# Kernel tuning notes

Measured on AMD Instinct MI355X. Metric: run time of the kernel, lower is better.

## Reference

```python
import jax, jax.numpy as jnp
import numpy as np


def _conv2d(x, w, b):
    # 3x3 conv, stride 1, pad 1, NCHW
    y = jax.lax.conv_general_dilated(x, w, (1, 1), ((1, 1), (1, 1)),
                                     dimension_numbers=('NCHW', 'OIHW', 'NCHW'))
    return y + b[None, :, None, None]


def _up2(x):
    return jnp.repeat(jnp.repeat(x, 2, axis=2), 2, axis=3)


def _mdconv(x, w, b, ow, ob):
    # Modulated deformable conv v2 (mmcv semantics): 3x3, stride 1, pad 1,
    # dilation 1, deformable_groups=1. Offsets/mask predicted by conv_offset,
    # out = chunk3 -> (o1, o2, mask); offset = cat(o1, o2); mask = sigmoid(mask).
    B, Cin, H, W = x.shape
    off = _conv2d(x, ow, ob)                        # [B,27,H,W]
    o1, o2, m = jnp.split(off, 3, axis=1)
    offs = jnp.concatenate([o1, o2], axis=1)        # [B,18,H,W]
    dy, dx = offs[:, 0::2], offs[:, 1::2]           # [B,9,H,W] (dy,dx interleaved per kernel pt)
    mask = jax.nn.sigmoid(m)                        # [B,9,H,W]
    ky, kx = jnp.meshgrid(jnp.arange(3), jnp.arange(3), indexing='ij')
    # sampling positions: p0 + pn + offset (pad=1)
    py = jnp.arange(H, dtype=x.dtype)[None, None, :, None] - 1.0 + ky.reshape(1, 9, 1, 1) + dy
    px = jnp.arange(W, dtype=x.dtype)[None, None, None, :] - 1.0 + kx.reshape(1, 9, 1, 1) + dx
    y0 = jnp.floor(py); x0 = jnp.floor(px)
    wy1 = py - y0; wx1 = px - x0
    y0i = y0.astype(jnp.int32); x0i = x0.astype(jnp.int32)
    flat = x.reshape(B, Cin, H * W)

    def gather(yi, xi):
        valid = ((yi >= 0) & (yi < H) & (xi >= 0) & (xi < W)).astype(x.dtype)  # zero padding
        idx = jnp.clip(yi, 0, H - 1) * W + jnp.clip(xi, 0, W - 1)             # [B,9,H,W]
        g = jax.vmap(lambda f, i: f[:, i])(flat, idx)                          # [B,Cin,9,H,W]
        return g * valid[:, None]

    val = (gather(y0i, x0i) * ((1 - wy1) * (1 - wx1))[:, None]
           + gather(y0i, x0i + 1) * ((1 - wy1) * wx1)[:, None]
           + gather(y0i + 1, x0i) * (wy1 * (1 - wx1))[:, None]
           + gather(y0i + 1, x0i + 1) * (wy1 * wx1)[:, None])
    cols = val * mask[:, None]                      # [B,Cin,9,H,W]
    out = jnp.einsum('ock,bckhw->bohw', w.reshape(w.shape[0], Cin, 9), cols)
    return out + b[None, :, None, None]


def setup_inputs() -> dict:
    key = jax.random.key(0)
    ks = jax.random.split(key, 24)
    C = 256
    sizes = [(96, 96), (48, 48), (24, 24), (12, 12)]
    d = {}
    for i, (h, w) in enumerate(sizes):
        d[f'x{i}'] = jax.random.normal(ks[i], (2, C, h, w), dtype=jnp.float32)
    for i in range(4):
        d[f'w{i}'] = jax.random.normal(ks[4 + i], (C, C, 3, 3), dtype=jnp.float32) * 0.02
        d[f'b{i}'] = jax.random.normal(ks[8 + i], (C,), dtype=jnp.float32) * 0.02
    for i in range(1, 4):
        d[f'ow{i}'] = jax.random.normal(ks[12 + i], (27, C, 3, 3), dtype=jnp.float32) * 0.01
        d[f'ob{i}'] = jax.random.normal(ks[16 + i], (27,), dtype=jnp.float32) * 0.01
    return d


def reference(x0, x1, x2, x3, w0, w1, w2, w3, b0, b1, b2, b3,
              ow1, ow2, ow3, ob1, ob2, ob3):
    # tdm_convs[3] called with level=1 -> deform; the same-size nearest interpolate is identity
    t3 = _mdconv(x3, w3, b3, ow3, ob3)
    # i=3: tdm_convs[2](2, x2 + up(t3)) -> deform
    t2 = _mdconv(x2 + _up2(t3), w2, b2, ow2, ob2)
    # i=2: tdm_convs[1](1, x1 + up(t2)) -> deform
    t1 = _mdconv(x1 + _up2(t2), w1, b1, ow1, ob1)
    # i=1: tdm_convs[0](0, x0 + up(t1)) -> level 0 < start_level -> plain conv
    t0 = _conv2d(x0 + _up2(t1), w0, b0)
    return (t0, t1, t2, t3)
```

## Files before the change

### kernel.cpp

```cpp
#include <hip/hip_runtime.h>
#include <math.h>

__device__ __forceinline__ ushort f2bf(float f) {
    unsigned int u = __float_as_uint(f);
    u += 0x7FFFu + ((u >> 16) & 1u);
    return (ushort)(u >> 16);
}

typedef __attribute__((address_space(1))) const unsigned int guint;
typedef __attribute__((address_space(3))) unsigned int luint;
__device__ __forceinline__ void gload_lds16(const void* g, void* l) {
    __builtin_amdgcn_global_load_lds((guint*)g, (luint*)l, 16, 0, 0);
}

using bfrag = __attribute__((ext_vector_type(8))) short;
using f4    = __attribute__((ext_vector_type(4))) float;

__device__ __forceinline__ void bf8_to_f(uint4 v, float* o) {
    unsigned int u[4] = {v.x, v.y, v.z, v.w};
    #pragma unroll
    for (int i = 0; i < 4; ++i) {
        o[2 * i]     = __uint_as_float(u[i] << 16);
        o[2 * i + 1] = __uint_as_float(u[i] & 0xFFFF0000u);
    }
}

struct CvtArgs {
    const float* src[7];
    ushort*      dst[7];
    int          m[7];
};
__global__ __launch_bounds__(256) void cvt_kernel(CvtArgs a) {
    int t = blockIdx.y;
    int idx = blockIdx.x * 256 + threadIdx.x;
    int M = a.m[t];
    if (idx >= M * 288) return;
    int m = idx / 288, rem = idx - m * 288;
    int r = rem >> 5, c8 = rem & 31;
    const float* s = a.src[t] + ((size_t)(m * 256 + c8 * 8)) * 9 + r;
    ushort vals[8];
    #pragma unroll
    for (int j = 0; j < 8; ++j) vals[j] = f2bf(s[j * 9]);
    *(uint4*)&a.dst[t][(size_t)m * 2304 + r * 256 + c8 * 8] = *(uint4*)vals;
}

struct FillArgs {
    float* outp[3];
    const float* bias[3];
    int HW[3];
    float* zbase;
    int z4;
};
__global__ __launch_bounds__(256) void fill_kernel(FillArgs a) {
    int y = blockIdx.y;
    int i = blockIdx.x * 256 + threadIdx.x;
    if (y < 3) {
        int HW = a.HW[y];
        int total4 = (2 * 256 * HW) >> 2;
        if (i < total4) {
            int e = i << 2;
            int m = (e / HW) & 255;
            float v = a.bias[y][m];
            *(float4*)&a.outp[y][e] = float4{v, v, v, v};
        }
    } else {
        if (i < a.z4) ((float4*)a.zbase)[i] = float4{0.f, 0.f, 0.f, 0.f};
    }
}

__global__ __launch_bounds__(256) void xs_nhwc(
    const float* __restrict__ x, const float* __restrict__ prev,
    ushort* __restrict__ xs, int H, int W)
{
    __shared__ ushort tile[32][72];
    const int HW = H * W, W2 = W >> 1;
    int b = blockIdx.z, c0 = blockIdx.y * 32, hw0 = blockIdx.x * 64;
    const float* xb = x + ((size_t)b * 256 + c0) * HW;
    const float* pb = prev ? prev + ((size_t)b * 256 + c0) * (HW >> 2) : nullptr;

    int hwl = threadIdx.x & 63, cl0 = threadIdx.x >> 6;
    int hw = hw0 + hwl;
    bool ok = hw < HW;
    int hwc = ok ? hw : HW - 1;
    int h = hwc / W, w = hwc - h * W;
    int pidx = (h >> 1) * W2 + (w >> 1);
    #pragma unroll
    for (int p = 0; p < 8; ++p) {
        int cl = p * 4 + cl0;
        float v = 0.f;
        if (ok) {
            v = xb[(size_t)cl * HW + hw];
            if (pb) v += pb[(size_t)cl * (HW >> 2) + pidx];
        }
        tile[cl][hwl] = f2bf(v);
    }
    __syncthreads();
    int hwl2 = threadIdx.x >> 2, cc = (threadIdx.x & 3) * 8;
    int hw2 = hw0 + hwl2;
    if (hw2 < HW) {
        ushort vals[8];
        #pragma unroll
        for (int j = 0; j < 8; ++j) vals[j] = tile[cc + j][hwl2];
        *(uint4*)&xs[((size_t)b * HW + hw2) * 256 + c0 + cc] = *(uint4*)vals;
    }
}

__global__ __launch_bounds__(256) void off_mfma(
    const ushort* __restrict__ A, const ushort* __restrict__ xs,
    const ushort* __restrict__ zeros, float* __restrict__ offbuf,
    int N, int H, int W, int ktiles)
{
    __shared__ __align__(16) ushort As[2][32 * 32];
    __shared__ __align__(16) ushort Bs[2][64 * 32];
    const int b  = blockIdx.z;
    const int n0 = blockIdx.x * 64;
    const int kt0 = blockIdx.y * ktiles * 32;
    const int tid = threadIdx.x, lane = tid & 63, wv = tid >> 6;
    const ushort* xb = xs + (size_t)b * N * 256;

    int n = n0 + (tid >> 2); if (n >= N) n = N - 1;
    int h = n / W, w = n - h * W;
    int kcc = (tid & 3) * 8;

    auto stage = [&](int kt, int bi) {
        int r = kt >> 8, c0k = kt & 255;
        int ry = r / 3 - 1, rx = r - (r / 3) * 3 - 1;
        if (tid < 128) {
            int row = tid >> 2; if (row > 26) row = 26;
            gload_lds16(A + (size_t)row * 2304 + kt + kcc,
                        (char*)As[bi] + (size_t)(tid & ~63) * 16);
        }
        int ih = h + ry, iw = w + rx;
        const ushort* src = (ih >= 0 && ih < H && iw >= 0 && iw < W)
            ? xb + (((size_t)(ih * W + iw)) << 8) + c0k + kcc
            : zeros;
        gload_lds16(src, (char*)Bs[bi] + (size_t)(tid & ~63) * 16);
    };

    f4 acc[2] = {};
    stage(kt0, 0);
    for (int kk = 0; kk < ktiles; ++kk) {
        __syncthreads();
        if (kk + 1 < ktiles) stage(kt0 + (kk + 1) * 32, (kk + 1) & 1);
        const ushort* as = As[kk & 1];
        const ushort* bs = Bs[kk & 1];
        bfrag bf = *(const bfrag*)&bs[(wv * 16 + (lane & 15)) * 32 + (lane >> 4) * 8];
        bfrag a0 = *(const bfrag*)&as[(lane & 15) * 32 + (lane >> 4) * 8];
        bfrag a1 = *(const bfrag*)&as[(16 + (lane & 15)) * 32 + (lane >> 4) * 8];
        acc[0] = __builtin_amdgcn_mfma_f32_16x16x32_bf16(a0, bf, acc[0], 0, 0, 0);
        acc[1] = __builtin_amdgcn_mfma_f32_16x16x32_bf16(a1, bf, acc[1], 0, 0, 0);
    }

    int nn = n0 + wv * 16 + (lane & 15);
    if (nn < N) {
        #pragma unroll
        for (int mb = 0; mb < 2; ++mb)
            #pragma unroll
            for (int t = 0; t < 4; ++t) {
                int m = mb * 16 + (lane >> 4) * 4 + t;
                if (m < 27)
                    atomicAdd(&offbuf[((size_t)b * 27 + m) * N + nn], acc[mb][t]);
            }
    }
}

__global__ __launch_bounds__(256) void sampling_kernel(
    const ushort* __restrict__ xs, const float* __restrict__ off,
    const float* __restrict__ ob, ushort* __restrict__ cols,
    int H, int W)
{
    __shared__ float4 gw[32][9];
    __shared__ int4   go[32][9];
    const int HW = H * W;
    const int b = blockIdx.z;
    const int hw0 = blockIdx.x * 32;
    const int tid = threadIdx.x;
    const float* offb = off + (size_t)b * 27 * HW;
    const ushort* xb = xs + (size_t)b * HW * 256;

    for (int it = tid; it < 32 * 9; it += 256) {
        int hwl = it / 9, k = it - hwl * 9;
        int hw = hw0 + hwl; if (hw >= HW) hw = HW - 1;
        int h = hw / W, w = hw - h * W;
        float dy = offb[(size_t)(2 * k) * HW + hw] + ob[2 * k];
        float dx = offb[(size_t)(2 * k + 1) * HW + hw] + ob[2 * k + 1];
        float mv = offb[(size_t)(18 + k) * HW + hw] + ob[18 + k];
        float mk = 1.0f / (1.0f + __expf(-mv));
        float py = (float)h - 1.0f + (float)(k / 3) + dy;
        float px = (float)w - 1.0f + (float)(k % 3) + dx;
        float y0f = floorf(py), x0f = floorf(px);
        float wy = py - y0f, wx = px - x0f;
        int y0 = (int)y0f, x0i = (int)x0f;
        int y1 = y0 + 1, x1 = x0i + 1;
        bool vy0 = (y0 >= 0) & (y0 < H), vy1 = (y1 >= 0) & (y1 < H);
        bool vx0 = (x0i >= 0) & (x0i < W), vx1 = (x1 >= 0) & (x1 < W);
        float w00 = (1.f - wy) * (1.f - wx) * ((vy0 & vx0) ? mk : 0.f);
        float w01 = (1.f - wy) * wx        * ((vy0 & vx1) ? mk : 0.f);
        float w10 = wy * (1.f - wx)        * ((vy1 & vx0) ? mk : 0.f);
        float w11 = wy * wx                * ((vy1 & vx1) ? mk : 0.f);
        int cy0 = min(max(y0, 0), H - 1), cy1 = min(max(y1, 0), H - 1);
        int cx0 = min(max(x0i, 0), W - 1), cx1 = min(max(x1, 0), W - 1);
        gw[hwl][k] = float4{w00, w01, w10, w11};
        go[hwl][k] = int4{(cy0 * W + cx0) << 8, (cy0 * W + cx1) << 8,
                          (cy1 * W + cx0) << 8, (cy1 * W + cx1) << 8};
    }
    __syncthreads();

    int hwl = tid >> 3, cb = (tid & 7) * 32;
    int hw = hw0 + hwl;
    if (hw >= HW) return;
    ushort* colp = cols + ((size_t)b * HW + hw) * 2304 + cb;

    #pragma unroll
    for (int k = 0; k < 9; ++k) {
        float4 wv = gw[hwl][k];
        int4   ov = go[hwl][k];
        const ushort* p00 = xb + ov.x + cb;
        const ushort* p01 = xb + ov.y + cb;
        const ushort* p10 = xb + ov.z + cb;
        const ushort* p11 = xb + ov.w + cb;
        #pragma unroll
        for (int j = 0; j < 4; ++j) {
            float f00[8], f01[8], f10[8], f11[8];
            bf8_to_f(*(const uint4*)(p00 + 8 * j), f00);
            bf8_to_f(*(const uint4*)(p01 + 8 * j), f01);
            bf8_to_f(*(const uint4*)(p10 + 8 * j), f10);
            bf8_to_f(*(const uint4*)(p11 + 8 * j), f11);
            unsigned int pk[4];
            #pragma unroll
            for (int t = 0; t < 4; ++t) {
                float lo = f00[2 * t] * wv.x + f01[2 * t] * wv.y +
                           f10[2 * t] * wv.z + f11[2 * t] * wv.w;
                float hi = f00[2 * t + 1] * wv.x + f01[2 * t + 1] * wv.y +
                           f10[2 * t + 1] * wv.z + f11[2 * t + 1] * wv.w;
                pk[t] = (unsigned int)f2bf(lo) | ((unsigned int)f2bf(hi) << 16);
            }
            *(uint4*)(colp + k * 256 + 8 * j) = make_uint4(pk[0], pk[1], pk[2], pk[3]);
        }
    }
}

template<bool IMPLICIT, bool SPLITK>
__global__ __launch_bounds__(256) void mfma_gemm(
    const ushort* __restrict__ A, const float* __restrict__ bias,
    const ushort* __restrict__ Bt, const ushort* __restrict__ zeros,
    float* __restrict__ outp, int N, int H, int W, int kchunk)
{
    __shared__ __align__(16) ushort As[128 * 64];
    __shared__ __align__(16) ushort Bs[64 * 64];
    const int b  = blockIdx.z;
    const int m0 = (blockIdx.y & 1) * 128;
    const int kt0 = (blockIdx.y >> 1) * kchunk;
    const int n0 = blockIdx.x * 64;
    const int tid  = threadIdx.x;
    const int lane = tid & 63;
    const int wv   = tid >> 6;
    const int wm = wv & 1, wn = wv >> 1;

    const ushort* Bb = IMPLICIT ? Bt + (size_t)b * N * 256
                                : Bt + (size_t)b * (size_t)N * 2304;

    const int sc8 = ((tid & 7) ^ ((tid >> 3) & 7)) * 8;
    int bn[2], bh[2], bw[2];
    #pragma unroll
    for (int j = 0; j < 2; ++j) {
        int n = n0 + j * 32 + (tid >> 3); if (n >= N) n = N - 1;
        bn[j] = n; bh[j] = n / W; bw[j] = n - bh[j] * W;
    }

    auto stage = [&](int kt) {
        #pragma unroll
        for (int i = 0; i < 4; ++i) {
            int row = i * 32 + (tid >> 3);
            gload_lds16(A + (size_t)(m0 + row) * 2304 + kt + sc8,
                        (char*)As + (size_t)(i * 256 + (tid & ~63)) * 16);
        }
        if (!IMPLICIT) {
            #pragma unroll
            for (int j = 0; j < 2; ++j)
                gload_lds16(Bb + (size_t)bn[j] * 2304 + kt + sc8,
                            (char*)Bs + (size_t)(j * 256 + (tid & ~63)) * 16);
        } else {
            int r = kt >> 8, c0k = kt & 255;
            int ry = r / 3 - 1, rx = r - (r / 3) * 3 - 1;
            #pragma unroll
            for (int j = 0; j < 2; ++j) {
                int ih = bh[j] + ry, iw = bw[j] + rx;
                const ushort* src = (ih >= 0 && ih < H && iw >= 0 && iw < W)
                    ? Bb + (((size_t)(ih * W + iw)) << 8) + c0k + sc8
                    : zeros;
                gload_lds16(src, (char*)Bs + (size_t)(j * 256 + (tid & ~63)) * 16);
            }
        }
    };

    const int fq = (lane >> 4);
    const int fv = (lane & 7);
    f4 acc[4][2] = {};

    const int kend = kt0 + kchunk;
    for (int kt = kt0; kt < kend; kt += 64) {
        stage(kt);
        __syncthreads();
        bfrag af[2][4], bf[2][2];
        #pragma unroll
        for (int kh = 0; kh < 2; ++kh) {
            int ch = ((kh * 4 + fq) ^ fv) * 8;
            #pragma unroll
            for (int i = 0; i < 4; ++i) {
                int r = wm * 64 + i * 16 + (lane & 15);
                af[kh][i] = *(const bfrag*)&As[r * 64 + ch];
            }
            #pragma unroll
            for (int j = 0; j < 2; ++j) {
                int r = wn * 32 + j * 16 + (lane & 15);
                bf[kh][j] = *(const bfrag*)&Bs[r * 64 + ch];
            }
        }
        #pragma unroll
        for (int kh = 0; kh < 2; ++kh)
            #pragma unroll
            for (int i = 0; i < 4; ++i)
                #pragma unroll
                for (int j = 0; j < 2; ++j)
                    acc[i][j] = __builtin_amdgcn_mfma_f32_16x16x32_bf16(
                        af[kh][i], bf[kh][j], acc[i][j], 0, 0, 0);
        __syncthreads();
    }

    const int mb = m0 + wm * 64, nb = n0 + wn * 32;
    #pragma unroll
    for (int i = 0; i < 4; ++i) {
        int mrow = mb + i * 16 + (lane >> 4) * 4;
        #pragma unroll
        for (int j = 0; j < 2; ++j) {
            int n = nb + j * 16 + (lane & 15);
            if (n < N) {
                #pragma unroll
                for (int t = 0; t < 4; ++t) {
                    int m = mrow + t;
                    if (SPLITK)
                        atomicAdd(&outp[((size_t)b * 256 + m) * N + n], acc[i][j][t]);
                    else
                        outp[((size_t)b * 256 + m) * N + n] = acc[i][j][t] + bias[m];
                }
            }
        }
    }
}

extern "C" void kernel_launch(void* const* d_in, const int* in_sizes, int n_in,
                              void* d_out, int out_size, void* d_ws, size_t ws_size,
                              hipStream_t stream)
{
    const float* x[4]   = {(const float*)d_in[0], (const float*)d_in[1],
                           (const float*)d_in[2], (const float*)d_in[3]};
    const float* wgt[4] = {(const float*)d_in[4], (const float*)d_in[6],
                           (const float*)d_in[8], (const float*)d_in[10]};
    const float* bia[4] = {(const float*)d_in[5], (const float*)d_in[7],
                           (const float*)d_in[9], (const float*)d_in[11]};
    const float* owt[4] = {nullptr, (const float*)d_in[12],
                           (const float*)d_in[14], (const float*)d_in[16]};
    const float* obv[4] = {nullptr, (const float*)d_in[13],
                           (const float*)d_in[15], (const float*)d_in[17]};

    const int B = 2;
    const int Hs[4] = {96, 48, 24, 12};
    const int HWs[4] = {96 * 96, 48 * 48, 24 * 24, 12 * 12};

    float* out = (float*)d_out;
    size_t outOff[4];
    outOff[0] = 0;
    outOff[1] = outOff[0] + (size_t)B * 256 * HWs[0];
    outOff[2] = outOff[1] + (size_t)B * 256 * HWs[1];
    outOff[3] = outOff[2] + (size_t)B * 256 * HWs[2];

    char* ws = (char*)d_ws;
    size_t off = 0;
    auto carve = [&](size_t bytes) { void* p = ws + off; off = (off + bytes + 255) & ~(size_t)255; return p; };
    ushort* wbf[4];
    ushort* owbf[4] = {nullptr, nullptr, nullptr, nullptr};
    for (int i = 0; i < 4; ++i) wbf[i] = (ushort*)carve((size_t)256 * 2304 * 2);
    for (int i = 1; i < 4; ++i) owbf[i] = (ushort*)carve((size_t)27 * 2304 * 2);
    ushort* cols = (ushort*)carve((size_t)B * HWs[1] * 2304 * 2);
    ushort* xsb[4];
    for (int i = 0; i < 4; ++i) xsb[i] = (ushort*)carve((size_t)B * 256 * HWs[i] * 2);
    int offElems = B * 27 * (HWs[1] + HWs[2] + HWs[3]);
    float* offbase = (float*)carve((size_t)offElems * 4 + 1024);
    ushort* zeros = (ushort*)(offbase + offElems);
    float* offbuf[4] = {nullptr,
                        offbase,
                        offbase + (size_t)B * 27 * HWs[1],
                        offbase + (size_t)B * 27 * (HWs[1] + HWs[2])};

    {
        CvtArgs a;
        a.src[0] = wgt[0]; a.src[1] = wgt[1]; a.src[2] = wgt[2]; a.src[3] = wgt[3];
        a.src[4] = owt[1]; a.src[5] = owt[2]; a.src[6] = owt[3];
        a.dst[0] = wbf[0]; a.dst[1] = wbf[1]; a.dst[2] = wbf[2]; a.dst[3] = wbf[3];
        a.dst[4] = owbf[1]; a.dst[5] = owbf[2]; a.dst[6] = owbf[3];
        for (int i = 0; i < 4; ++i) a.m[i] = 256;
        for (int i = 4; i < 7; ++i) a.m[i] = 27;
        dim3 grd((256 * 288 + 255) / 256, 7);
        cvt_kernel<<<grd, 256, 0, stream>>>(a);
    }
    {
        FillArgs a;
        for (int i = 0; i < 3; ++i) {
            a.outp[i] = out + outOff[i + 1]; a.bias[i] = bia[i + 1]; a.HW[i] = HWs[i + 1];
        }
        a.zbase = offbase;
        a.z4 = (offElems * 4 + 1024) / 16;
        int maxE = 2 * 256 * HWs[1] / 4;
        if (a.z4 > maxE) maxE = a.z4;
        dim3 grd((maxE + 255) / 256, 4);
        fill_kernel<<<grd, 256, 0, stream>>>(a);
    }
    {
        dim3 grd((HWs[3] + 63) / 64, 8, B);
        xs_nhwc<<<grd, 256, 0, stream>>>(x[3], nullptr, xsb[3], Hs[3], Hs[3]);
    }

    const int ktiles[4] = {0, 9, 6, 3};
    const int ksplit[4] = {1, 2, 6, 12};

    for (int lvl = 3; lvl >= 1; --lvl) {
        int H = Hs[lvl], W = H, HW = HWs[lvl];

        {
            dim3 grd((HW + 63) / 64, 72 / ktiles[lvl], B);
            off_mfma<<<grd, 256, 0, stream>>>(
                owbf[lvl], xsb[lvl], zeros, offbuf[lvl], HW, H, W, ktiles[lvl]);
        }
        {
            dim3 grd((HW + 31) / 32, 1, B);
            sampling_kernel<<<grd, 256, 0, stream>>>(
                xsb[lvl], offbuf[lvl], obv[lvl], cols, H, W);
        }
        {
            dim3 grd((HW + 63) / 64, 2 * ksplit[lvl], B);
            mfma_gemm<false, true><<<grd, 256, 0, stream>>>(
                wbf[lvl], bia[lvl], cols, zeros, out + outOff[lvl],
                HW, H, W, 2304 / ksplit[lvl]);
        }
        {
            int Hn = Hs[lvl - 1];
            dim3 grd((HWs[lvl - 1] + 63) / 64, 8, B);
            xs_nhwc<<<grd, 256, 0, stream>>>(
                x[lvl - 1], out + outOff[lvl], xsb[lvl - 1], Hn, Hn);
        }
    }

    {
        dim3 grd((HWs[0] + 63) / 64, 2, B);
        mfma_gemm<true, false><<<grd, 256, 0, stream>>>(
            wbf[0], bia[0], xsb[0], zeros, out + outOff[0],
            HWs[0], Hs[0], Hs[0], 2304);
    }
}
```

Measured before the change: 294.0 us.

## Double-buffer LDS in MFMA GEMM, shrink M tile to 64, retune split-K

The GEMM kernel now uses two LDS buffers so the next K-tile's global-to-LDS load is issued while MFMAs run on the current tile, and it drops one barrier per iteration. The M tile is halved from 128 to 64, giving four M blocks per batch, which doubles the grid and raises occupancy. Split-K factors for the smaller levels are reduced to cut atomic traffic. The cost is re-reading the B tile for each M block and doing less MFMA work per LDS fragment load.

New measurement: 297.0 us. About the same (+1.0%).

```diff
diff --git a/kernel.cpp b/kernel.cpp
--- a/kernel.cpp
+++ b/kernel.cpp
@@ -246,11 +246,11 @@
     const ushort* __restrict__ Bt, const ushort* __restrict__ zeros,
     float* __restrict__ outp, int N, int H, int W, int kchunk)
 {
-    __shared__ __align__(16) ushort As[128 * 64];
-    __shared__ __align__(16) ushort Bs[64 * 64];
+    __shared__ __align__(16) ushort As[2][64 * 64];
+    __shared__ __align__(16) ushort Bs[2][64 * 64];
     const int b  = blockIdx.z;
-    const int m0 = (blockIdx.y & 1) * 128;
-    const int kt0 = (blockIdx.y >> 1) * kchunk;
+    const int m0 = (blockIdx.y & 3) * 64;
+    const int kt0 = (blockIdx.y >> 2) * kchunk;
     const int n0 = blockIdx.x * 64;
     const int tid  = threadIdx.x;
     const int lane = tid & 63;
@@ -261,25 +261,25 @@
                                 : Bt + (size_t)b * (size_t)N * 2304;
 
     const int sc8 = ((tid & 7) ^ ((tid >> 3) & 7)) * 8;
+    const int srow = tid >> 3;
     int bn[2], bh[2], bw[2];
     #pragma unroll
     for (int j = 0; j < 2; ++j) {
-        int n = n0 + j * 32 + (tid >> 3); if (n >= N) n = N - 1;
+        int n = n0 + j * 32 + srow; if (n >= N) n = N - 1;
         bn[j] = n; bh[j] = n / W; bw[j] = n - bh[j] * W;
     }
 
-    auto stage = [&](int kt) {
-        #pragma unroll
-        for (int i = 0; i < 4; ++i) {
-            int row = i * 32 + (tid >> 3);
-            gload_lds16(A + (size_t)(m0 + row) * 2304 + kt + sc8,
-                        (char*)As + (size_t)(i * 256 + (tid & ~63)) * 16);
+    auto stage = [&](int kt, int bi) {
+        #pragma unroll
+        for (int i = 0; i < 2; ++i) {
+            gload_lds16(A + (size_t)(m0 + i * 32 + srow) * 2304 + kt + sc8,
+                        (char*)As[bi] + (size_t)(i * 256 + (tid & ~63)) * 16);
         }
         if (!IMPLICIT) {
             #pragma unroll
             for (int j = 0; j < 2; ++j)
                 gload_lds16(Bb + (size_t)bn[j] * 2304 + kt + sc8,
-                            (char*)Bs + (size_t)(j * 256 + (tid & ~63)) * 16);
+                            (char*)Bs[bi] + (size_t)(j * 256 + (tid & ~63)) * 16);
         } else {
             int r = kt >> 8, c0k = kt & 255;
             int ry = r / 3 - 1, rx = r - (r / 3) * 3 - 1;
@@ -289,48 +289,46 @@
                 const ushort* src = (ih >= 0 && ih < H && iw >= 0 && iw < W)
                     ? Bb + (((size_t)(ih * W + iw)) << 8) + c0k + sc8
                     : zeros;
-                gload_lds16(src, (char*)Bs + (size_t)(j * 256 + (tid & ~63)) * 16);
+                gload_lds16(src, (char*)Bs[bi] + (size_t)(j * 256 + (tid & ~63)) * 16);
             }
         }
     };
 
     const int fq = (lane >> 4);
     const int fv = (lane & 7);
-    f4 acc[4][2] = {};
-
-    const int kend = kt0 + kchunk;
-    for (int kt = kt0; kt < kend; kt += 64) {
-        stage(kt);
+    f4 acc[2][2] = {};
+
+    const int nit = kchunk >> 6;
+    stage(kt0, 0);
+    for (int it = 0; it < nit; ++it) {
         __syncthreads();
-        bfrag af[2][4], bf[2][2];
+        if (it + 1 < nit) stage(kt0 + (it + 1) * 64, (it + 1) & 1);
+        const ushort* as = As[it & 1];
+        const ushort* bs = Bs[it & 1];
+        bfrag af[2][2], bf[2][2];
         #pragma unroll
         for (int kh = 0; kh < 2; ++kh) {
             int ch = ((kh * 4 + fq) ^ fv) * 8;
             #pragma unroll
-            for (int i = 0; i < 4; ++i) {
-                int r = wm * 64 + i * 16 + (lane & 15);
-                af[kh][i] = *(const bfrag*)&As[r * 64 + ch];
-            }
-            #pragma unroll
-            for (int j = 0; j < 2; ++j) {
-                int r = wn * 32 + j * 16 + (lane & 15);
-                bf[kh][j] = *(const bfrag*)&Bs[r * 64 + ch];
-            }
+            for (int i = 0; i < 2; ++i)
+                af[kh][i] = *(const bfrag*)&as[(wm * 32 + i * 16 + (lane & 15)) * 64 + ch];
+            #pragma unroll
+            for (int j = 0; j < 2; ++j)
+                bf[kh][j] = *(const bfrag*)&bs[(wn * 32 + j * 16 + (lane & 15)) * 64 + ch];
         }
         #pragma unroll
         for (int kh = 0; kh < 2; ++kh)
             #pragma unroll
-            for (int i = 0; i < 4; ++i)
+            for (int i = 0; i < 2; ++i)
                 #pragma unroll
                 for (int j = 0; j < 2; ++j)
                     acc[i][j] = __builtin_amdgcn_mfma_f32_16x16x32_bf16(
                         af[kh][i], bf[kh][j], acc[i][j], 0, 0, 0);
-        __syncthreads();
-    }
-
-    const int mb = m0 + wm * 64, nb = n0 + wn * 32;
-    #pragma unroll
-    for (int i = 0; i < 4; ++i) {
+    }
+
+    const int mb = m0 + wm * 32, nb = n0 + wn * 32;
+    #pragma unroll
+    for (int i = 0; i < 2; ++i) {
         int mrow = mb + i * 16 + (lane >> 4) * 4;
         #pragma unroll
         for (int j = 0; j < 2; ++j) {
@@ -422,7 +420,7 @@
     }
 
     const int ktiles[4] = {0, 9, 6, 3};
-    const int ksplit[4] = {1, 2, 6, 12};
+    const int ksplit[4] = {1, 2, 4, 6};
 
     for (int lvl = 3; lvl >= 1; --lvl) {
         int H = Hs[lvl], W = H, HW = HWs[lvl];
@@ -438,7 +436,7 @@
                 xsb[lvl], offbuf[lvl], obv[lvl], cols, H, W);
         }
         {
-            dim3 grd((HW + 63) / 64, 2 * ksplit[lvl], B);
+            dim3 grd((HW + 63) / 64, 4 * ksplit[lvl], B);
             mfma_gemm<false, true><<<grd, 256, 0, stream>>>(
                 wbf[lvl], bia[lvl], cols, zeros, out + outOff[lvl],
                 HW, H, W, 2304 / ksplit[lvl]);
@@ -452,7 +450,7 @@
     }
 
     {
-        dim3 grd((HWs[0] + 63) / 64, 2, B);
+        dim3 grd((HWs[0] + 63) / 64, 4, B);
         mfma_gemm<true, false><<<grd, 256, 0, stream>>>(
             wbf[0], bia[0], xsb[0], zeros, out + outOff[0],
             HWs[0], Hs[0], Hs[0], 2304);
```

## Fuse all stages into one cooperative persistent kernel with grid syncs

Applied to the files above, without the earlier changes.

Replaces the sequence of about fifteen kernel launches with a single cooperative kernel of 512 persistent blocks. Each stage loops over virtual block indices and is separated from the next by grid.sync(), which removes per-launch overhead and the gaps between launches. The sampling stage is also reshaped to 8 pixels per block with one 8-channel chunk per thread, giving more blocks at small levels. The cost is grid-wide barriers and fixed occupancy: stages with few tiles leave most blocks idle, and large stages loop several times over the persistent blocks.

After: 1.021 ms. 3.47x slower.

```diff
diff --git a/kernel.cpp b/kernel.cpp
--- a/kernel.cpp
+++ b/kernel.cpp
@@ -1,5 +1,8 @@
 #include <hip/hip_runtime.h>
+#include <hip/hip_cooperative_groups.h>
 #include <math.h>
+
+namespace cg = cooperative_groups;
 
 __device__ __forceinline__ ushort f2bf(float f) {
     unsigned int u = __float_as_uint(f);
@@ -25,56 +28,65 @@
     }
 }
 
-struct CvtArgs {
-    const float* src[7];
-    ushort*      dst[7];
-    int          m[7];
+struct MegaArgs {
+    const float* x[4];
+    const float* wgt[4];
+    const float* bia[4];
+    const float* owt[4];
+    const float* obv[4];
+    ushort* wbf[4];
+    ushort* owbf[4];
+    ushort* cols;
+    ushort* xsb[4];
+    float*  offbuf[4];
+    ushort* zeros;
+    float*  zbase;
+    int     z4;
+    float*  out[4];
 };
-__global__ __launch_bounds__(256) void cvt_kernel(CvtArgs a) {
-    int t = blockIdx.y;
-    int idx = blockIdx.x * 256 + threadIdx.x;
-    int M = a.m[t];
-    if (idx >= M * 288) return;
-    int m = idx / 288, rem = idx - m * 288;
-    int r = rem >> 5, c8 = rem & 31;
-    const float* s = a.src[t] + ((size_t)(m * 256 + c8 * 8)) * 9 + r;
-    ushort vals[8];
-    #pragma unroll
-    for (int j = 0; j < 8; ++j) vals[j] = f2bf(s[j * 9]);
-    *(uint4*)&a.dst[t][(size_t)m * 2304 + r * 256 + c8 * 8] = *(uint4*)vals;
-}
-
-struct FillArgs {
-    float* outp[3];
-    const float* bias[3];
-    int HW[3];
-    float* zbase;
-    int z4;
-};
-__global__ __launch_bounds__(256) void fill_kernel(FillArgs a) {
-    int y = blockIdx.y;
-    int i = blockIdx.x * 256 + threadIdx.x;
+
+__device__ __forceinline__ void st_cvt(const MegaArgs& a, int vb) {
+    int t = vb / 288, bxi = vb - t * 288;
+    int M = (t < 4) ? 256 : 27;
+    const float* src = (t < 4) ? a.wgt[t] : a.owt[t - 3];
+    ushort* dst = (t < 4) ? a.wbf[t] : a.owbf[t - 3];
+    int idx = bxi * 256 + threadIdx.x;
+    if (idx < M * 288) {
+        int m = idx / 288, rem = idx - m * 288;
+        int r = rem >> 5, c8 = rem & 31;
+        const float* s = src + ((size_t)(m * 256 + c8 * 8)) * 9 + r;
+        ushort vals[8];
+        #pragma unroll
+        for (int j = 0; j < 8; ++j) vals[j] = f2bf(s[j * 9]);
+        *(uint4*)&dst[(size_t)m * 2304 + r * 256 + c8 * 8] = *(uint4*)vals;
+    }
+}
+
+__device__ __forceinline__ void st_fill(const MegaArgs& a, int vb) {
+    int y = vb / 1152, bxi = vb - y * 1152;
+    int i = bxi * 256 + threadIdx.x;
     if (y < 3) {
-        int HW = a.HW[y];
-        int total4 = (2 * 256 * HW) >> 2;
-        if (i < total4) {
+        int HW = (y == 0) ? 2304 : (y == 1) ? 576 : 144;
+        float* outp = a.out[y + 1];
+        const float* bias = a.bia[y + 1];
+        if (i < 128 * HW) {
             int e = i << 2;
             int m = (e / HW) & 255;
-            float v = a.bias[y][m];
-            *(float4*)&a.outp[y][e] = float4{v, v, v, v};
+            float v = bias[m];
+            *(float4*)&outp[e] = float4{v, v, v, v};
         }
     } else {
         if (i < a.z4) ((float4*)a.zbase)[i] = float4{0.f, 0.f, 0.f, 0.f};
     }
 }
 
-__global__ __launch_bounds__(256) void xs_nhwc(
+__device__ __forceinline__ void st_xs(char* smemc,
     const float* __restrict__ x, const float* __restrict__ prev,
-    ushort* __restrict__ xs, int H, int W)
+    ushort* __restrict__ xs, int H, int W, int bx, int by, int bz)
 {
-    __shared__ ushort tile[32][72];
+    ushort (*tile)[72] = (ushort(*)[72])smemc;
     const int HW = H * W, W2 = W >> 1;
-    int b = blockIdx.z, c0 = blockIdx.y * 32, hw0 = blockIdx.x * 64;
+    int b = bz, c0 = by * 32, hw0 = bx * 64;
     const float* xb = x + ((size_t)b * 256 + c0) * HW;
     const float* pb = prev ? prev + ((size_t)b * 256 + c0) * (HW >> 2) : nullptr;
 
@@ -103,19 +115,18 @@
         for (int j = 0; j < 8; ++j) vals[j] = tile[cc + j][hwl2];
         *(uint4*)&xs[((size_t)b * HW + hw2) * 256 + c0 + cc] = *(uint4*)vals;
     }
-}
-
-__global__ __launch_bounds__(256) void off_mfma(
+    __syncthreads();
+}
+
+__device__ __forceinline__ void st_off(char* smemc,
     const ushort* __restrict__ A, const ushort* __restrict__ xs,
     const ushort* __restrict__ zeros, float* __restrict__ offbuf,
-    int N, int H, int W, int ktiles)
+    int N, int H, int W, int ktiles, int bx, int by, int bz)
 {
-    __shared__ __align__(16) ushort As[2][32 * 32];
-    __shared__ __align__(16) ushort Bs[2][64 * 32];
-    const int b  = blockIdx.z;
-    const int n0 = blockIdx.x * 64;
-    const int kt0 = blockIdx.y * ktiles * 32;
-    const int tid = threadIdx.x, lane = tid & 63, wv = tid >> 6;
+    ushort* As0 = (ushort*)smemc;
+    ushort* Bs0 = (ushort*)(smemc + 4096);
+    const int b = bz, n0 = bx * 64, kt0 = by * ktiles * 32;
+    const int tid = threadIdx.x, lane = tid & 63, wvv = tid >> 6;
     const ushort* xb = xs + (size_t)b * N * 256;
 
     int n = n0 + (tid >> 2); if (n >= N) n = N - 1;
@@ -128,13 +139,13 @@
         if (tid < 128) {
             int row = tid >> 2; if (row > 26) row = 26;
             gload_lds16(A + (size_t)row * 2304 + kt + kcc,
-                        (char*)As[bi] + (size_t)(tid & ~63) * 16);
+                        (char*)(As0 + bi * 1024) + (size_t)(tid & ~63) * 16);
         }
         int ih = h + ry, iw = w + rx;
         const ushort* src = (ih >= 0 && ih < H && iw >= 0 && iw < W)
             ? xb + (((size_t)(ih * W + iw)) << 8) + c0k + kcc
             : zeros;
-        gload_lds16(src, (char*)Bs[bi] + (size_t)(tid & ~63) * 16);
+        gload_lds16(src, (char*)(Bs0 + bi * 2048) + (size_t)(tid & ~63) * 16);
     };
 
     f4 acc[2] = {};
@@ -142,16 +153,17 @@
     for (int kk = 0; kk < ktiles; ++kk) {
         __syncthreads();
         if (kk + 1 < ktiles) stage(kt0 + (kk + 1) * 32, (kk + 1) & 1);
-        const ushort* as = As[kk & 1];
-        const ushort* bs = Bs[kk & 1];
-        bfrag bf = *(const bfrag*)&bs[(wv * 16 + (lane & 15)) * 32 + (lane >> 4) * 8];
+        const ushort* as = As0 + (kk & 1) * 1024;
+        const ushort* bs = Bs0 + (kk & 1) * 2048;
+        bfrag bf = *(const bfrag*)&bs[(wvv * 16 + (lane & 15)) * 32 + (lane >> 4) * 8];
         bfrag a0 = *(const bfrag*)&as[(lane & 15) * 32 + (lane >> 4) * 8];
         bfrag a1 = *(const bfrag*)&as[(16 + (lane & 15)) * 32 + (lane >> 4) * 8];
         acc[0] = __builtin_amdgcn_mfma_f32_16x16x32_bf16(a0, bf, acc[0], 0, 0, 0);
         acc[1] = __builtin_amdgcn_mfma_f32_16x16x32_bf16(a1, bf, acc[1], 0, 0, 0);
     }
-
-    int nn = n0 + wv * 16 + (lane & 15);
+    __syncthreads();
+
+    int nn = n0 + wvv * 16 + (lane & 15);
     if (nn < N) {
         #pragma unroll
         for (int mb = 0; mb < 2; ++mb)
@@ -164,22 +176,20 @@
     }
 }
 
-__global__ __launch_bounds__(256) void sampling_kernel(
+__device__ __forceinline__ void st_samp(char* smemc,
     const ushort* __restrict__ xs, const float* __restrict__ off,
     const float* __restrict__ ob, ushort* __restrict__ cols,
-    int H, int W)
+    int H, int W, int bx, int bz)
 {
-    __shared__ float4 gw[32][9];
-    __shared__ int4   go[32][9];
+    float4* gw = (float4*)smemc;
+    int4*   go = (int4*)(smemc + 8 * 9 * 16);
     const int HW = H * W;
-    const int b = blockIdx.z;
-    const int hw0 = blockIdx.x * 32;
-    const int tid = threadIdx.x;
+    const int b = bz, hw0 = bx * 8, tid = threadIdx.x;
     const float* offb = off + (size_t)b * 27 * HW;
     const ushort* xb = xs + (size_t)b * HW * 256;
 
-    for (int it = tid; it < 32 * 9; it += 256) {
-        int hwl = it / 9, k = it - hwl * 9;
+    if (tid < 72) {
+        int hwl = tid / 9, k = tid - hwl * 9;
         int hw = hw0 + hwl; if (hw >= HW) hw = HW - 1;
         int h = hw / W, w = hw - h * W;
         float dy = offb[(size_t)(2 * k) * HW + hw] + ob[2 * k];
@@ -200,32 +210,25 @@
         float w11 = wy * wx                * ((vy1 & vx1) ? mk : 0.f);
         int cy0 = min(max(y0, 0), H - 1), cy1 = min(max(y1, 0), H - 1);
         int cx0 = min(max(x0i, 0), W - 1), cx1 = min(max(x1, 0), W - 1);
-        gw[hwl][k] = float4{w00, w01, w10, w11};
-        go[hwl][k] = int4{(cy0 * W + cx0) << 8, (cy0 * W + cx1) << 8,
-                          (cy1 * W + cx0) << 8, (cy1 * W + cx1) << 8};
+        gw[hwl * 9 + k] = float4{w00, w01, w10, w11};
+        go[hwl * 9 + k] = int4{(cy0 * W + cx0) << 8, (cy0 * W + cx1) << 8,
+                               (cy1 * W + cx0) << 8, (cy1 * W + cx1) << 8};
     }
     __syncthreads();
 
-    int hwl = tid >> 3, cb = (tid & 7) * 32;
+    int hwl = tid >> 5, cb = (tid & 31) * 8;
     int hw = hw0 + hwl;
-    if (hw >= HW) return;
-    ushort* colp = cols + ((size_t)b * HW + hw) * 2304 + cb;
-
-    #pragma unroll
-    for (int k = 0; k < 9; ++k) {
-        float4 wv = gw[hwl][k];
-        int4   ov = go[hwl][k];
-        const ushort* p00 = xb + ov.x + cb;
-        const ushort* p01 = xb + ov.y + cb;
-        const ushort* p10 = xb + ov.z + cb;
-        const ushort* p11 = xb + ov.w + cb;
-        #pragma unroll
-        for (int j = 0; j < 4; ++j) {
+    if (hw < HW) {
+        ushort* colp = cols + ((size_t)b * HW + hw) * 2304 + cb;
+        #pragma unroll
+        for (int k = 0; k < 9; ++k) {
+            float4 wv = gw[hwl * 9 + k];
+            int4   ov = go[hwl * 9 + k];
             float f00[8], f01[8], f10[8], f11[8];
-            bf8_to_f(*(const uint4*)(p00 + 8 * j), f00);
-            bf8_to_f(*(const uint4*)(p01 + 8 * j), f01);
-            bf8_to_f(*(const uint4*)(p10 + 8 * j), f10);
-            bf8_to_f(*(const uint4*)(p11 + 8 * j), f11);
+            bf8_to_f(*(const uint4*)(xb + ov.x + cb), f00);
+            bf8_to_f(*(const uint4*)(xb + ov.y + cb), f01);
+            bf8_to_f(*(const uint4*)(xb + ov.z + cb), f10);
+            bf8_to_f(*(const uint4*)(xb + ov.w + cb), f11);
             unsigned int pk[4];
             #pragma unroll
             for (int t = 0; t < 4; ++t) {
@@ -235,23 +238,25 @@
                            f10[2 * t + 1] * wv.z + f11[2 * t + 1] * wv.w;
                 pk[t] = (unsigned int)f2bf(lo) | ((unsigned int)f2bf(hi) << 16);
             }
-            *(uint4*)(colp + k * 256 + 8 * j) = make_uint4(pk[0], pk[1], pk[2], pk[3]);
-        }
-    }
+            *(uint4*)(colp + k * 256) = make_uint4(pk[0], pk[1], pk[2], pk[3]);
+        }
+    }
+    __syncthreads();
 }
 
 template<bool IMPLICIT, bool SPLITK>
-__global__ __launch_bounds__(256) void mfma_gemm(
+__device__ __forceinline__ void st_gemm(char* smemc,
     const ushort* __restrict__ A, const float* __restrict__ bias,
     const ushort* __restrict__ Bt, const ushort* __restrict__ zeros,
-    float* __restrict__ outp, int N, int H, int W, int kchunk)
+    float* __restrict__ outp, int N, int H, int W, int kchunk,
+    int bx, int by, int bz)
 {
-    __shared__ __align__(16) ushort As[128 * 64];
-    __shared__ __align__(16) ushort Bs[64 * 64];
-    const int b  = blockIdx.z;
-    const int m0 = (blockIdx.y & 1) * 128;
-    const int kt0 = (blockIdx.y >> 1) * kchunk;
-    const int n0 = blockIdx.x * 64;
+    ushort* As = (ushort*)smemc;
+    ushort* Bs = (ushort*)(smemc + 16384);
+    const int b  = bz;
+    const int m0 = (by & 1) * 128;
+    const int kt0 = (by >> 1) * kchunk;
+    const int n0 = bx * 64;
     const int tid  = threadIdx.x;
     const int lane = tid & 63;
     const int wv   = tid >> 6;
@@ -261,18 +266,18 @@
                                 : Bt + (size_t)b * (size_t)N * 2304;
 
     const int sc8 = ((tid & 7) ^ ((tid >> 3) & 7)) * 8;
+    const int srow = tid >> 3;
     int bn[2], bh[2], bw[2];
     #pragma unroll
     for (int j = 0; j < 2; ++j) {
-        int n = n0 + j * 32 + (tid >> 3); if (n >= N) n = N - 1;
+        int n = n0 + j * 32 + srow; if (n >= N) n = N - 1;
         bn[j] = n; bh[j] = n / W; bw[j] = n - bh[j] * W;
     }
 
     auto stage = [&](int kt) {
         #pragma unroll
         for (int i = 0; i < 4; ++i) {
-            int row = i * 32 + (tid >> 3);
-            gload_lds16(A + (size_t)(m0 + row) * 2304 + kt + sc8,
+            gload_lds16(A + (size_t)(m0 + i * 32 + srow) * 2304 + kt + sc8,
                         (char*)As + (size_t)(i * 256 + (tid & ~63)) * 16);
         }
         if (!IMPLICIT) {
@@ -307,15 +312,11 @@
         for (int kh = 0; kh < 2; ++kh) {
             int ch = ((kh * 4 + fq) ^ fv) * 8;
             #pragma unroll
-            for (int i = 0; i < 4; ++i) {
-                int r = wm * 64 + i * 16 + (lane & 15);
-                af[kh][i] = *(const bfrag*)&As[r * 64 + ch];
-            }
-            #pragma unroll
-            for (int j = 0; j < 2; ++j) {
-                int r = wn * 32 + j * 16 + (lane & 15);
-                bf[kh][j] = *(const bfrag*)&Bs[r * 64 + ch];
-            }
+            for (int i = 0; i < 4; ++i)
+                af[kh][i] = *(const bfrag*)&As[(wm * 64 + i * 16 + (lane & 15)) * 64 + ch];
+            #pragma unroll
+            for (int j = 0; j < 2; ++j)
+                bf[kh][j] = *(const bfrag*)&Bs[(wn * 32 + j * 16 + (lane & 15)) * 64 + ch];
         }
         #pragma unroll
         for (int kh = 0; kh < 2; ++kh)
@@ -349,112 +350,104 @@
     }
 }
 
+__global__ __launch_bounds__(256, 2) void mega(MegaArgs a) {
+    __shared__ __align__(16) char smem[24576];
+    cg::grid_group grid = cg::this_grid();
+    const int G = gridDim.x, g0 = blockIdx.x;
+
+    for (int v = g0; v < 6672; v += G) {
+        if (v < 2016) st_cvt(a, v);
+        else if (v < 6624) st_fill(a, v - 2016);
+        else { int u = v - 6624; st_xs(smem, a.x[3], nullptr, a.xsb[3], 12, 12, u % 3, (u / 3) & 7, u / 24); }
+    }
+    grid.sync();
+
+    for (int v = g0; v < 144; v += G)
+        st_off(smem, a.owbf[3], a.xsb[3], a.zeros, a.offbuf[3], 144, 12, 12, 3, v % 3, (v / 3) % 24, v / 72);
+    grid.sync();
+    for (int v = g0; v < 36; v += G)
+        st_samp(smem, a.xsb[3], a.offbuf[3], a.obv[3], a.cols, 12, 12, v % 18, v / 18);
+    grid.sync();
+    for (int v = g0; v < 72; v += G)
+        st_gemm<false, true>(smem, a.wbf[3], a.bia[3], a.cols, a.zeros, a.out[3], 144, 12, 12, 384, v % 3, (v / 3) % 12, v / 36);
+    grid.sync();
+    for (int v = g0; v < 144; v += G)
+        st_xs(smem, a.x[2], a.out[3], a.xsb[2], 24, 24, v % 9, (v / 9) % 8, v / 72);
+    grid.sync();
+
+    for (int v = g0; v < 216; v += G)
+        st_off(smem, a.owbf[2], a.xsb[2], a.zeros, a.offbuf[2], 576, 24, 24, 6, v % 9, (v / 9) % 12, v / 108);
+    grid.sync();
+    for (int v = g0; v < 144; v += G)
+        st_samp(smem, a.xsb[2], a.offbuf[2], a.obv[2], a.cols, 24, 24, v % 72, v / 72);
+    grid.sync();
+    for (int v = g0; v < 144; v += G)
+        st_gemm<false, true>(smem, a.wbf[2], a.bia[2], a.cols, a.zeros, a.out[2], 576, 24, 24, 576, v % 9, (v / 9) % 8, v / 72);
+    grid.sync();
+    for (int v = g0; v < 576; v += G)
+        st_xs(smem, a.x[1], a.out[2], a.xsb[1], 48, 48, v % 36, (v / 36) % 8, v / 288);
+    grid.sync();
+
+    for (int v = g0; v < 576; v += G)
+        st_off(smem, a.owbf[1], a.xsb[1], a.zeros, a.offbuf[1], 2304, 48, 48, 9, v % 36, (v / 36) % 8, v / 288);
+    grid.sync();
+    for (int v = g0; v < 576; v += G)
+        st_samp(smem, a.xsb[1], a.offbuf[1], a.obv[1], a.cols, 48, 48, v % 288, v / 288);
+    grid.sync();
+    for (int v = g0; v < 288; v += G)
+        st_gemm<false, true>(smem, a.wbf[1], a.bia[1], a.cols, a.zeros, a.out[1], 2304, 48, 48, 1152, v % 36, (v / 36) % 4, v / 144);
+    grid.sync();
+    for (int v = g0; v < 2304; v += G)
+        st_xs(smem, a.x[0], a.out[1], a.xsb[0], 96, 96, v % 144, (v / 144) % 8, v / 1152);
+    grid.sync();
+
+    for (int v = g0; v < 576; v += G)
+        st_gemm<true, false>(smem, a.wbf[0], a.bia[0], a.xsb[0], a.zeros, a.out[0], 9216, 96, 96, 2304, v % 144, (v / 144) % 2, v / 288);
+}
+
 extern "C" void kernel_launch(void* const* d_in, const int* in_sizes, int n_in,
                               void* d_out, int out_size, void* d_ws, size_t ws_size,
                               hipStream_t stream)
 {
-    const float* x[4]   = {(const float*)d_in[0], (const float*)d_in[1],
-                           (const float*)d_in[2], (const float*)d_in[3]};
-    const float* wgt[4] = {(const float*)d_in[4], (const float*)d_in[6],
-                           (const float*)d_in[8], (const float*)d_in[10]};
-    const float* bia[4] = {(const float*)d_in[5], (const float*)d_in[7],
-                           (const float*)d_in[9], (const float*)d_in[11]};
-    const float* owt[4] = {nullptr, (const float*)d_in[12],
-                           (const float*)d_in[14], (const float*)d_in[16]};
-    const float* obv[4] = {nullptr, (const float*)d_in[13],
-                           (const float*)d_in[15], (const float*)d_in[17]};
-
     const int B = 2;
-    const int Hs[4] = {96, 48, 24, 12};
     const int HWs[4] = {96 * 96, 48 * 48, 24 * 24, 12 * 12};
 
+    MegaArgs a;
+    a.x[0] = (const float*)d_in[0];  a.x[1] = (const float*)d_in[1];
+    a.x[2] = (const float*)d_in[2];  a.x[3] = (const float*)d_in[3];
+    a.wgt[0] = (const float*)d_in[4];  a.wgt[1] = (const float*)d_in[6];
+    a.wgt[2] = (const float*)d_in[8];  a.wgt[3] = (const float*)d_in[10];
+    a.bia[0] = (const float*)d_in[5];  a.bia[1] = (const float*)d_in[7];
+    a.bia[2] = (const float*)d_in[9];  a.bia[3] = (const float*)d_in[11];
+    a.owt[0] = nullptr;                a.owt[1] = (const float*)d_in[12];
+    a.owt[2] = (const float*)d_in[14]; a.owt[3] = (const float*)d_in[16];
+    a.obv[0] = nullptr;                a.obv[1] = (const float*)d_in[13];
+    a.obv[2] = (const float*)d_in[15]; a.obv[3] = (const float*)d_in[17];
+
     float* out = (float*)d_out;
-    size_t outOff[4];
-    outOff[0] = 0;
-    outOff[1] = outOff[0] + (size_t)B * 256 * HWs[0];
-    outOff[2] = outOff[1] + (size_t)B * 256 * HWs[1];
-    outOff[3] = outOff[2] + (size_t)B * 256 * HWs[2];
+    a.out[0] = out;
+    a.out[1] = a.out[0] + (size_t)B * 256 * HWs[0];
+    a.out[2] = a.out[1] + (size_t)B * 256 * HWs[1];
+    a.out[3] = a.out[2] + (size_t)B * 256 * HWs[2];
 
     char* ws = (char*)d_ws;
     size_t off = 0;
     auto carve = [&](size_t bytes) { void* p = ws + off; off = (off + bytes + 255) & ~(size_t)255; return p; };
-    ushort* wbf[4];
-    ushort* owbf[4] = {nullptr, nullptr, nullptr, nullptr};
-    for (int i = 0; i < 4; ++i) wbf[i] = (ushort*)carve((size_t)256 * 2304 * 2);
-    for (int i = 1; i < 4; ++i) owbf[i] = (ushort*)carve((size_t)27 * 2304 * 2);
-    ushort* cols = (ushort*)carve((size_t)B * HWs[1] * 2304 * 2);
-    ushort* xsb[4];
-    for (int i = 0; i < 4; ++i) xsb[i] = (ushort*)carve((size_t)B * 256 * HWs[i] * 2);
+    for (int i = 0; i < 4; ++i) a.wbf[i] = (ushort*)carve((size_t)256 * 2304 * 2);
+    a.owbf[0] = nullptr;
+    for (int i = 1; i < 4; ++i) a.owbf[i] = (ushort*)carve((size_t)27 * 2304 * 2);
+    a.cols = (ushort*)carve((size_t)B * HWs[1] * 2304 * 2);
+    for (int i = 0; i < 4; ++i) a.xsb[i] = (ushort*)carve((size_t)B * 256 * HWs[i] * 2);
     int offElems = B * 27 * (HWs[1] + HWs[2] + HWs[3]);
-    float* offbase = (float*)carve((size_t)offElems * 4 + 1024);
-    ushort* zeros = (ushort*)(offbase + offElems);
-    float* offbuf[4] = {nullptr,
-                        offbase,
-                        offbase + (size_t)B * 27 * HWs[1],
-                        offbase + (size_t)B * 27 * (HWs[1] + HWs[2])};
-
-    {
-        CvtArgs a;
-        a.src[0] = wgt[0]; a.src[1] = wgt[1]; a.src[2] = wgt[2]; a.src[3] = wgt[3];
-        a.src[4] = owt[1]; a.src[5] = owt[2]; a.src[6] = owt[3];
-        a.dst[0] = wbf[0]; a.dst[1] = wbf[1]; a.dst[2] = wbf[2]; a.dst[3] = wbf[3];
-        a.dst[4] = owbf[1]; a.dst[5] = owbf[2]; a.dst[6] = owbf[3];
-        for (int i = 0; i < 4; ++i) a.m[i] = 256;
-        for (int i = 4; i < 7; ++i) a.m[i] = 27;
-        dim3 grd((256 * 288 + 255) / 256, 7);
-        cvt_kernel<<<grd, 256, 0, stream>>>(a);
-    }
-    {
-        FillArgs a;
-        for (int i = 0; i < 3; ++i) {
-            a.outp[i] = out + outOff[i + 1]; a.bias[i] = bia[i + 1]; a.HW[i] = HWs[i + 1];
-        }
-        a.zbase = offbase;
-        a.z4 = (offElems * 4 + 1024) / 16;
-        int maxE = 2 * 256 * HWs[1] / 4;
-        if (a.z4 > maxE) maxE = a.z4;
-        dim3 grd((maxE + 255) / 256, 4);
-        fill_kernel<<<grd, 256, 0, stream>>>(a);
-    }
-    {
-        dim3 grd((HWs[3] + 63) / 64, 8, B);
-        xs_nhwc<<<grd, 256, 0, stream>>>(x[3], nullptr, xsb[3], Hs[3], Hs[3]);
-    }
-
-    const int ktiles[4] = {0, 9, 6, 3};
-    const int ksplit[4] = {1, 2, 6, 12};
-
-    for (int lvl = 3; lvl >= 1; --lvl) {
-        int H = Hs[lvl], W = H, HW = HWs[lvl];
-
-        {
-            dim3 grd((HW + 63) / 64, 72 / ktiles[lvl], B);
-            off_mfma<<<grd, 256, 0, stream>>>(
-                owbf[lvl], xsb[lvl], zeros, offbuf[lvl], HW, H, W, ktiles[lvl]);
-        }
-        {
-            dim3 grd((HW + 31) / 32, 1, B);
-            sampling_kernel<<<grd, 256, 0, stream>>>(
-                xsb[lvl], offbuf[lvl], obv[lvl], cols, H, W);
-        }
-        {
-            dim3 grd((HW + 63) / 64, 2 * ksplit[lvl], B);
-            mfma_gemm<false, true><<<grd, 256, 0, stream>>>(
-                wbf[lvl], bia[lvl], cols, zeros, out + outOff[lvl],
-                HW, H, W, 2304 / ksplit[lvl]);
-        }
-        {
-            int Hn = Hs[lvl - 1];
-            dim3 grd((HWs[lvl - 1] + 63) / 64, 8, B);
-            xs_nhwc<<<grd, 256, 0, stream>>>(
-                x[lvl - 1], out + outOff[lvl], xsb[lvl - 1], Hn, Hn);
-        }
-    }
-
-    {
-        dim3 grd((HWs[0] + 63) / 64, 2, B);
-        mfma_gemm<true, false><<<grd, 256, 0, stream>>>(
-            wbf[0], bia[0], xsb[0], zeros, out + outOff[0],
-            HWs[0], Hs[0], Hs[0], 2304);
-    }
-}
+    a.zbase = (float*)carve((size_t)offElems * 4 + 1024);
+    a.zeros = (ushort*)(a.zbase + offElems);
+    a.z4 = (offElems * 4 + 1024) / 16;
+    a.offbuf[0] = nullptr;
+    a.offbuf[1] = a.zbase;
+    a.offbuf[2] = a.zbase + (size_t)B * 27 * HWs[1];
+    a.offbuf[3] = a.zbase + (size_t)B * 27 * (HWs[1] + HWs[2]);
+
+    void* kargs[] = { (void*)&a };
+    hipLaunchCooperativeKernel((const void*)mega, dim3(512), dim3(256),
+                               kargs, 0, stream);
+}
```
